# Optimization experiments

Hardware: AMD Instinct MI355X
Metric: run time of the kernel (lower is better)

The kernel has to match this reference:

```python
import jax, jax.numpy as jnp
import numpy as np

B, TM1, E, D = 512, 256, 256, 256  # batch, T-1, encoder_hidden, decoder_hidden


def setup_inputs() -> dict:
    key = jax.random.key(0)
    ks = jax.random.split(key, 10)
    s = 0.05
    return {
        "input_encoded": jax.random.normal(ks[0], (B, TM1, E), dtype=jnp.float32),
        "y_history": jax.random.normal(ks[1], (B, TM1, 1), dtype=jnp.float32),
        # attn_layer: Linear(2D+E -> E), Tanh, Linear(E -> 1)
        "attn_w1": jax.random.normal(ks[2], (E, 2 * D + E), dtype=jnp.float32) * s,
        "attn_b1": jnp.zeros((E,), jnp.float32),
        "attn_w2": jax.random.normal(ks[3], (1, E), dtype=jnp.float32) * s,
        "attn_b2": jnp.zeros((1,), jnp.float32),
        # LSTM cell: input_size=1, hidden=D
        "W_ih": jax.random.normal(ks[4], (4 * D, 1), dtype=jnp.float32) * s,
        "W_hh": jax.random.normal(ks[5], (4 * D, D), dtype=jnp.float32) * s,
        "b_ih": jnp.zeros((4 * D,), jnp.float32),
        "b_hh": jnp.zeros((4 * D,), jnp.float32),
        # fc: Linear(E+1 -> 1), weight init normal_()
        "fc_w": jax.random.normal(ks[6], (1, E + 1), dtype=jnp.float32),
        "fc_b": jnp.zeros((1,), jnp.float32),
        # fc_final: Linear(D+E -> 2) (probabilistic)
        "fcf_w": jax.random.normal(ks[7], (2, D + E), dtype=jnp.float32) * s,
        "fcf_b": jnp.zeros((2,), jnp.float32),
    }


def _forward(input_encoded, y_history, attn_w1, attn_b1, attn_w2, attn_b2,
             W_ih, W_hh, b_ih, b_hh, fc_w, fc_b, fcf_w, fcf_b):
    # Split attn first linear into [hidden|cell] part and encoder part.
    w1_hc = attn_w1[:, : 2 * D]   # (E, 2D)
    w1_enc = attn_w1[:, 2 * D:]   # (E, E)
    # Encoder projection is invariant across timesteps: compute once. (B,TM1,E)
    enc_proj = jnp.einsum("bte,fe->btf", input_encoded, w1_enc) + attn_b1

    def step(carry, y_t):
        h, c, _ = carry  # h,c: (B,D); y_t: (B,1)
        hc = jnp.concatenate([h, c], axis=1)                     # (B, 2D)
        pre = jnp.tanh(enc_proj + (hc @ w1_hc.T)[:, None, :])    # (B, TM1, E)
        scores = jnp.einsum("bte,oe->bto", pre, attn_w2)[..., 0] + attn_b2[0]  # (B, TM1)
        alpha = jax.nn.softmax(scores, axis=1)
        context = jnp.einsum("bt,bte->be", alpha, input_encoded)  # (B, E)
        y_tilde = jnp.concatenate([context, y_t], axis=1) @ fc_w.T + fc_b  # (B,1)
        # LSTM cell (torch gate order: i, f, g, o)
        gates = y_tilde @ W_ih.T + b_ih + h @ W_hh.T + b_hh  # (B, 4D)
        i, f, g, o = jnp.split(gates, 4, axis=1)
        i = jax.nn.sigmoid(i); f = jax.nn.sigmoid(f)
        g = jnp.tanh(g); o = jax.nn.sigmoid(o)
        c_new = f * c + i * g
        h_new = o * jnp.tanh(c_new)
        return (h_new, c_new, context), None

    h0 = jnp.zeros((input_encoded.shape[0], D), input_encoded.dtype)
    c0 = jnp.zeros_like(h0)
    ctx0 = jnp.zeros((input_encoded.shape[0], E), input_encoded.dtype)
    ys = jnp.transpose(y_history, (1, 0, 2))  # (TM1, B, 1)
    (h, c, context), _ = jax.lax.scan(step, (h0, c0, ctx0), ys)
    return jnp.concatenate([h, context], axis=1) @ fcf_w.T + fcf_b  # (B, 2)


def reference(input_encoded, y_history, attn_w1, attn_b1, attn_w2, attn_b2,
              W_ih, W_hh, b_ih, b_hh, fc_w, fc_b, fcf_w, fcf_b):
    return _forward(input_encoded, y_history, attn_w1, attn_b1, attn_w2, attn_b2,
                    W_ih, W_hh, b_ih, b_hh, fc_w, fc_b, fcf_w, fcf_b)
```

## Files before the change

### kernel.cpp

```cpp
#include <hip/hip_runtime.h>
#include <cstdint>
#include <cstddef>


typedef _Float16 half8 __attribute__((ext_vector_type(8)));
typedef _Float16 half4v __attribute__((ext_vector_type(4)));
typedef _Float16 half2v __attribute__((ext_vector_type(2)));

__device__ __forceinline__ float rcpf_(float x) { return __builtin_amdgcn_rcpf(x); }
__device__ __forceinline__ float sigmoidf_(float x) { return rcpf_(1.f + __expf(-x)); }
__device__ __forceinline__ float tanhf_(float x) { return 1.f - 2.f * rcpf_(1.f + __expf(2.f * x)); }

#if defined(__has_builtin)
#if __has_builtin(__builtin_amdgcn_fdot2)
#define HAS_FDOT2 1
#endif
#endif
#ifndef HAS_FDOT2
#define HAS_FDOT2 0
#endif

__device__ __forceinline__ float fdot2_(half2v a, half2v b, float c) {
#if HAS_FDOT2
  return __builtin_amdgcn_fdot2(a, b, c, false);
#else
  return fmaf((float)a[0], (float)b[0], fmaf((float)a[1], (float)b[1], c));
#endif
}

__device__ __forceinline__ float dot8_(half8 w, half8 h, float acc) {
  acc = fdot2_(__builtin_shufflevector(w, w, 0, 1), __builtin_shufflevector(h, h, 0, 1), acc);
  acc = fdot2_(__builtin_shufflevector(w, w, 2, 3), __builtin_shufflevector(h, h, 2, 3), acc);
  acc = fdot2_(__builtin_shufflevector(w, w, 4, 5), __builtin_shufflevector(h, h, 4, 5), acc);
  acc = fdot2_(__builtin_shufflevector(w, w, 6, 7), __builtin_shufflevector(h, h, 6, 7), acc);
  return acc;
}


__global__ void k_prep_wT(const float* __restrict__ w1, float* __restrict__ wT) {
  int id = blockIdx.x * 256 + threadIdx.x;
  int e = id >> 8, f = id & 255;
  wT[id] = w1[f * 768 + 512 + e];
}

__global__ void k_prep_xh(const float* __restrict__ x, _Float16* __restrict__ xh) {
  int id = blockIdx.x * 256 + threadIdx.x;
  float4 v = reinterpret_cast<const float4*>(x)[id];
  half4v h;
  h[0] = (_Float16)v.x; h[1] = (_Float16)v.y; h[2] = (_Float16)v.z; h[3] = (_Float16)v.w;
  reinterpret_cast<half4v*>(xh)[id] = h;
}

__global__ void k_prep_w1hcQ(const float* __restrict__ w1, _Float16* __restrict__ o) {
  int id = blockIdx.x * 256 + threadIdx.x;
  int m = id & 7, lane = (id >> 3) & 511, c = id >> 12;
  int e = lane >> 1, kh = lane & 1;
  o[id] = (_Float16)w1[e * 768 + kh * 256 + c * 8 + m];
}

__global__ void k_prep_whhG(const float* __restrict__ whh, _Float16* __restrict__ o) {
  int id = blockIdx.x * 256 + threadIdx.x;
  int m = id & 7, j = (id >> 3) & 1023, c = id >> 13;
  o[id] = (_Float16)whh[j * 256 + c * 8 + m];
}

__global__ __launch_bounds__(256) void k_xf(const float* __restrict__ x,
                                            const float* __restrict__ fcw,
                                            float* __restrict__ xf) {
  __shared__ float xl[16][256];
  __shared__ float fw[256];
  __shared__ float part[16][17];
  const int tid = threadIdx.x;
  const int m0 = blockIdx.x * 16;
  fw[tid] = fcw[tid];
#pragma unroll
  for (int r = 0; r < 16; ++r) xl[r][tid] = x[(size_t)(m0 + r) * 256 + tid];
  __syncthreads();
  int r = tid >> 4, p = tid & 15;
  float s = 0.f;
#pragma unroll
  for (int u = 0; u < 16; ++u) s = fmaf(xl[r][p * 16 + u], fw[p * 16 + u], s);
  part[r][p] = s;
  __syncthreads();
  if (tid < 16) {
    float t = 0.f;
#pragma unroll
    for (int p2 = 0; p2 < 16; ++p2) t += part[tid][p2];
    xf[m0 + tid] = t;
  }
}

__global__ __launch_bounds__(256) void k_encp(const float* __restrict__ x,
                                              const float* __restrict__ wT,
                                              const float* __restrict__ b1,
                                              _Float16* __restrict__ Ph2) {
  __shared__ __align__(16) float xl[16][256];
  const int tid = threadIdx.x;
  const int m0 = blockIdx.x * 16;
#pragma unroll
  for (int r = 0; r < 16; ++r) xl[r][tid] = x[(size_t)(m0 + r) * 256 + tid];
  __syncthreads();
  float acc[16];
#pragma unroll
  for (int r = 0; r < 16; ++r) acc[r] = 0.f;
  for (int e = 0; e < 256; e += 4) {
    float w0 = wT[(e + 0) * 256 + tid];
    float w1_ = wT[(e + 1) * 256 + tid];
    float w2_ = wT[(e + 2) * 256 + tid];
    float w3_ = wT[(e + 3) * 256 + tid];
#pragma unroll
    for (int r = 0; r < 16; ++r) {
      float4 xv = *reinterpret_cast<const float4*>(&xl[r][e]);
      acc[r] = fmaf(xv.x, w0, acc[r]);
      acc[r] = fmaf(xv.y, w1_, acc[r]);
      acc[r] = fmaf(xv.z, w2_, acc[r]);
      acc[r] = fmaf(xv.w, w3_, acc[r]);
    }
  }
  float bb = b1[tid];
  const int e = tid;
#pragma unroll
  for (int r = 0; r < 16; ++r) {
    int m = m0 + r, b = m >> 8, t = m & 255;
    float p = __expf(2.f * (acc[r] + bb));
    Ph2[((size_t)(b * 32 + (e >> 3)) * 256 + t) * 8 + (e & 7)] = (_Float16)p;
  }
}

#define SC1(pv, c) { \
  float4 qa = q4[2*(c)], wa = w4[2*(c)]; \
  sacc0 = fmaf(wa.x, rcpf_(fmaf((float)pv[0], qa.x, 1.f)), sacc0); \
  sacc1 = fmaf(wa.y, rcpf_(fmaf((float)pv[1], qa.y, 1.f)), sacc1); \
  sacc0 = fmaf(wa.z, rcpf_(fmaf((float)pv[2], qa.z, 1.f)), sacc0); \
  sacc1 = fmaf(wa.w, rcpf_(fmaf((float)pv[3], qa.w, 1.f)), sacc1); \
  float4 qb = q4[2*(c)+1], wb = w4[2*(c)+1]; \
  sacc0 = fmaf(wb.x, rcpf_(fmaf((float)pv[4], qb.x, 1.f)), sacc0); \
  sacc1 = fmaf(wb.y, rcpf_(fmaf((float)pv[5], qb.y, 1.f)), sacc1); \
  sacc0 = fmaf(wb.z, rcpf_(fmaf((float)pv[6], qb.z, 1.f)), sacc0); \
  sacc1 = fmaf(wb.w, rcpf_(fmaf((float)pv[7], qb.w, 1.f)), sacc1); }

__global__ __launch_bounds__(1024, 4) void k_scan(
    const _Float16* __restrict__ Ph2, const _Float16* __restrict__ xh,
    const _Float16* __restrict__ w1hcQ, const _Float16* __restrict__ whhG,
    const float* __restrict__ xf, const float* __restrict__ y_hist,
    const float* __restrict__ w2g, const float* __restrict__ Wih,
    const float* __restrict__ bih, const float* __restrict__ bhh,
    const float* __restrict__ fcw, const float* __restrict__ fcb,
    const float* __restrict__ fcfw, const float* __restrict__ fcfb,
    float* __restrict__ out) {
  __shared__ __align__(16) float hc[2][512];
  __shared__ __align__(16) _Float16 hcH[2][512];
  __shared__ __align__(16) float Qs[2][256];
  __shared__ __align__(16) float spart[2][2][256];
  __shared__ __align__(16) float ealpha[2][256];
  __shared__ __align__(16) float gfull[2][1024];
  __shared__ __align__(16) _Float16 PhL[2][14][256][8];
  __shared__ __align__(16) float w2l[256];
  __shared__ __align__(16) float Wihl[1024];
  __shared__ __align__(16) float bl[1024];
  __shared__ __align__(16) float xfL[2][256];
  __shared__ __align__(16) float yhL[2][256];
  __shared__ float redA[8], redB[8];

  const int tid = threadIdx.x;
  const int b0 = blockIdx.x * 2;
  const int lo = tid & 255;
  const int wv = tid >> 6, lane = tid & 63;

  ((float*)hc)[tid] = 0.f;
  ((_Float16*)hcH)[tid] = (_Float16)0.f;
  if (tid < 256) w2l[tid] = w2g[tid];
  Wihl[tid & 1023] = Wih[tid & 1023];
  bl[tid] = bih[tid] + bhh[tid];
  if (tid < 512) {
    int gi = tid >> 8, ti = tid & 255;
    xfL[gi][ti] = xf[(size_t)(b0 + gi) * 256 + ti];
    yhL[gi][ti] = y_hist[(size_t)(b0 + gi) * 256 + ti];
  }
  {
    half8* phl8 = reinterpret_cast<half8*>(&PhL[0][0][0][0]);
    const half8* ph8 = reinterpret_cast<const half8*>(Ph2);
#pragma unroll
    for (int u2 = 0; u2 < 7; ++u2) {
      int slot = u2 * 1024 + tid;
      int g = slot >= 3584;
      int rem = slot - g * 3584;
      int ci = rem >> 8;
      int t = rem & 255;
      int cc = (ci < 7) ? (2 * ci) : (16 + 2 * (ci - 7));
      phl8[slot] = ph8[((size_t)(b0 + g) * 32 + cc) * 256 + t];
    }
  }
  __syncthreads();
  float w2sum = 0.f;
  for (int e2 = 0; e2 < 256; ++e2) w2sum += w2l[e2];
  const float fcb0 = fcb[0];
  const float fcwy = fcw[256];

  const half8* wq2 = reinterpret_cast<const half8*>(w1hcQ) + tid;
  const int khq = tid & 1;
  const int ug = (tid - 512) & 511;
  const half8* wgJ = reinterpret_cast<const half8*>(whhG) + ug;
  const int gs = tid >> 9, eh = (tid >> 8) & 1;
  const half8* prow = reinterpret_cast<const half8*>(Ph2) +
                      ((size_t)((b0 + gs) * 32 + eh * 16)) * 256 + lo;
  const half8* phlR = reinterpret_cast<const half8*>(&PhL[0][0][0][0]) +
                      (gs * 14 + eh * 7) * 256 + lo;
  const int gp = (tid >> 8) & 1;

#pragma unroll 1
  for (int s = 0; s < 256; ++s) {
    if (tid < 512) {
      float a0 = 0.f, a1 = 0.f;
      const half8* hp0 = reinterpret_cast<const half8*>(&hcH[0][khq * 256]);
      const half8* hp1 = reinterpret_cast<const half8*>(&hcH[1][khq * 256]);
#pragma unroll 8
      for (int c = 0; c < 32; ++c) {
        half8 w = wq2[c * 512];
        a0 = dot8_(w, hp0[c], a0);
        a1 = dot8_(w, hp1[c], a1);
      }
      a0 += __shfl_xor(a0, 1);
      a1 += __shfl_xor(a1, 1);
      if (khq == 0) {
        int e = tid >> 1;
        Qs[0][e] = __expf(2.f * a0);
        Qs[1][e] = __expf(2.f * a1);
      }
    } else {
      float ac00 = 0.f, ac01 = 0.f, ac10 = 0.f, ac11 = 0.f;
      const half8* hg0 = reinterpret_cast<const half8*>(&hcH[0][0]);
      const half8* hg1 = reinterpret_cast<const half8*>(&hcH[1][0]);
#pragma unroll 4
      for (int c = 0; c < 32; ++c) {
        half8 h0 = hg0[c];
        half8 h1 = hg1[c];
        half8 w0 = wgJ[c * 1024];
        half8 w1v = wgJ[c * 1024 + 512];
        ac00 = dot8_(w0, h0, ac00);  ac01 = dot8_(w0, h1, ac01);
        ac10 = dot8_(w1v, h0, ac10); ac11 = dot8_(w1v, h1, ac11);
      }
      gfull[0][ug] = ac00;
      gfull[1][ug] = ac01;
      gfull[0][ug + 512] = ac10;
      gfull[1][ug + 512] = ac11;
    }
    __syncthreads();

    float sacc0 = 0.f, sacc1 = 0.f;
    {
      const float4* q4 = reinterpret_cast<const float4*>(&Qs[gs][eh * 128]);
      const float4* w4 = reinterpret_cast<const float4*>(&w2l[eh * 128]);
      half8 s1 = prow[1 * 256];
      half8 s3 = prow[3 * 256];
      half8 s5 = prow[5 * 256];
      half8 s7 = prow[7 * 256];
      half8 s9 = prow[9 * 256];
      half8 s11 = prow[11 * 256];
      half8 s13 = prow[13 * 256];
      half8 s14 = prow[14 * 256];
      half8 s15 = prow[15 * 256];
      { half8 l0 = phlR[0 * 256];  SC1(l0, 0) }
      { half8 l2 = phlR[1 * 256];  SC1(l2, 2) }
      { half8 l4 = phlR[2 * 256];  SC1(l4, 4) }
      { half8 l6 = phlR[3 * 256];  SC1(l6, 6) }
      { half8 l8 = phlR[4 * 256];  SC1(l8, 8) }
      { half8 la = phlR[5 * 256];  SC1(la, 10) }
      { half8 lc = phlR[6 * 256];  SC1(lc, 12) }
      SC1(s1, 1)  SC1(s3, 3)  SC1(s5, 5)  SC1(s7, 7)  SC1(s9, 9)
      SC1(s11, 11) SC1(s13, 13) SC1(s14, 14) SC1(s15, 15)
    }
    spart[eh][gs][lo] = sacc0 + sacc1;
    __syncthreads();

    if (tid < 512) {
      float sc = w2sum - 2.f * (spart[0][gp][lo] + spart[1][gp][lo]);
      float ea = __expf(sc);
      ealpha[gp][lo] = ea;
      float ef = ea * xfL[gp][lo];
      float es = ea;
#pragma unroll
      for (int off = 32; off > 0; off >>= 1) {
        es += __shfl_xor(es, off);
        ef += __shfl_xor(ef, off);
      }
      if (lane == 0) { redA[wv] = es; redB[wv] = ef; }
    }
    __syncthreads();

    if (tid < 512) {
      float es = (gp == 0) ? (redA[0] + redA[1] + redA[2] + redA[3])
                           : (redA[4] + redA[5] + redA[6] + redA[7]);
      float ef = (gp == 0) ? (redB[0] + redB[1] + redB[2] + redB[3])
                           : (redB[4] + redB[5] + redB[6] + redB[7]);
      float yt = ef * rcpf_(es) + fmaf(yhL[gp][s], fcwy, fcb0);
      float gi = fmaf(yt, Wihl[lo], bl[lo]) + gfull[gp][lo];
      float gf = fmaf(yt, Wihl[256 + lo], bl[256 + lo]) + gfull[gp][256 + lo];
      float gc = fmaf(yt, Wihl[512 + lo], bl[512 + lo]) + gfull[gp][512 + lo];
      float go = fmaf(yt, Wihl[768 + lo], bl[768 + lo]) + gfull[gp][768 + lo];
      float iv = sigmoidf_(gi), fv = sigmoidf_(gf), gv = tanhf_(gc), ov = sigmoidf_(go);
      float cold = hc[gp][256 + lo];
      float cn = fmaf(fv, cold, iv * gv);
      float hn = ov * tanhf_(cn);
      hc[gp][lo] = hn;
      hc[gp][256 + lo] = cn;
      hcH[gp][lo] = (_Float16)hn;
      hcH[gp][256 + lo] = (_Float16)cn;
    }
    __syncthreads();
  }

  const float rsA = rcpf_(redA[0] + redA[1] + redA[2] + redA[3]);
  const float rsB = rcpf_(redA[4] + redA[5] + redA[6] + redA[7]);

  float* cpartF = reinterpret_cast<float*>(&PhL[0][0][0][0]);
  {
    const int gc = tid >> 9, t16 = (tid >> 5) & 15, l5 = tid & 31;
    const half8* xrow = reinterpret_cast<const half8*>(xh) +
                        ((size_t)(b0 + gc) * 256 + t16 * 16) * 32 + l5;
    float acx[8];
#pragma unroll
    for (int m = 0; m < 8; ++m) acx[m] = 0.f;
#pragma unroll 4
    for (int it = 0; it < 16; ++it) {
      float al = ealpha[gc][t16 * 16 + it];
      half8 xv = xrow[it * 32];
#pragma unroll
      for (int m = 0; m < 8; ++m) acx[m] = fmaf(al, (float)xv[m], acx[m]);
    }
    float* dst = &cpartF[((gc * 16 + t16) * 256) + l5 * 8];
    *reinterpret_cast<float4*>(dst) = *reinterpret_cast<float4*>(&acx[0]);
    *reinterpret_cast<float4*>(dst + 4) = *reinterpret_cast<float4*>(&acx[4]);
  }
  __syncthreads();

  if (tid < 512) {
    float cv = 0.f;
#pragma unroll
    for (int u = 0; u < 16; ++u) cv += cpartF[((gp * 16 + u) * 256) + lo];
    cv *= (gp == 0) ? rsA : rsB;
    float hval = hc[gp][lo];
    float p0 = hval * fcfw[lo] + cv * fcfw[256 + lo];
    float p1 = hval * fcfw[512 + lo] + cv * fcfw[768 + lo];
#pragma unroll
    for (int off = 32; off > 0; off >>= 1) {
      p0 += __shfl_xor(p0, off);
      p1 += __shfl_xor(p1, off);
    }
    if (lane == 0) { redA[wv] = p0; redB[wv] = p1; }
  }
  __syncthreads();
  if (tid < 4) {
    int g2 = tid >> 1, o = tid & 1;
    const float* r = (o == 0) ? redA : redB;
    float v = fcfb[o] + r[g2 * 4 + 0] + r[g2 * 4 + 1] + r[g2 * 4 + 2] + r[g2 * 4 + 3];
    out[(b0 + g2) * 2 + o] = v;
  }
}

extern "C" void kernel_launch(void* const* d_in, const int* in_sizes, int n_in,
                              void* d_out, int out_size, void* d_ws, size_t ws_size,
                              hipStream_t stream) {
  (void)in_sizes; (void)n_in; (void)out_size; (void)ws_size;
  const float* x    = (const float*)d_in[0];
  const float* yh   = (const float*)d_in[1];
  const float* w1   = (const float*)d_in[2];
  const float* b1   = (const float*)d_in[3];
  const float* w2   = (const float*)d_in[4];
  const float* Wih  = (const float*)d_in[6];
  const float* Whh  = (const float*)d_in[7];
  const float* bih  = (const float*)d_in[8];
  const float* bhh  = (const float*)d_in[9];
  const float* fcw  = (const float*)d_in[10];
  const float* fcb  = (const float*)d_in[11];
  const float* fcfw = (const float*)d_in[12];
  const float* fcfb = (const float*)d_in[13];
  float* out = (float*)d_out;

  char* ws = (char*)d_ws;
  _Float16* Ph2   = (_Float16*)(ws);
  _Float16* xh    = (_Float16*)(ws + (size_t)67108864);
  float*    wT    = (float*)   (ws + (size_t)134217728);
  _Float16* w1hcQ = (_Float16*)(ws + (size_t)134479872);
  _Float16* whhG  = (_Float16*)(ws + (size_t)134742016);
  float*    xf    = (float*)   (ws + (size_t)135266304);

  k_prep_wT   <<<256,   256, 0, stream>>>(w1, wT);
  k_prep_xh   <<<32768, 256, 0, stream>>>(x, xh);
  k_prep_w1hcQ<<<512,   256, 0, stream>>>(w1, w1hcQ);
  k_prep_whhG <<<1024,  256, 0, stream>>>(Whh, whhG);
  k_xf        <<<8192,  256, 0, stream>>>(x, fcw, xf);
  k_encp      <<<8192,  256, 0, stream>>>(x, wT, b1, Ph2);
  k_scan      <<<256,  1024, 0, stream>>>(Ph2, xh, w1hcQ, whhG, xf, yh, w2, Wih,
                                          bih, bhh, fcw, fcb, fcfw, fcfb, out);
}
```

Measured before the change: 3.722 ms.

## Overlap attention scores with split W_hh gate matvec across thread halves

The W_hh gate matvec is split into two halves. The second half now runs on the upper 512 threads at the same time as the attention-score pass, which is done entirely by the lower 512 threads over all 256 encoder features. This removes the spart partial-score buffer and one block barrier per timestep. The LDS copy of the projected encoder is widened to hold all even chunks, and the c half of hcH is padded to reduce bank conflicts. In exchange, each score thread does twice as much rcp-heavy work and issues more global loads, which lengthens the score critical path and pushes LDS use close to the limit.

```diff
diff --git a/kernel.cpp b/kernel.cpp
--- a/kernel.cpp
+++ b/kernel.cpp
@@ -149,12 +149,11 @@
     const float* __restrict__ fcfw, const float* __restrict__ fcfb,
     float* __restrict__ out) {
   __shared__ __align__(16) float hc[2][512];
-  __shared__ __align__(16) _Float16 hcH[2][512];
+  __shared__ __align__(16) _Float16 hcH[2][520];
   __shared__ __align__(16) float Qs[2][256];
-  __shared__ __align__(16) float spart[2][2][256];
   __shared__ __align__(16) float ealpha[2][256];
   __shared__ __align__(16) float gfull[2][1024];
-  __shared__ __align__(16) _Float16 PhL[2][14][256][8];
+  __shared__ __align__(16) _Float16 PhL[2][16][256][8];
   __shared__ __align__(16) float w2l[256];
   __shared__ __align__(16) float Wihl[1024];
   __shared__ __align__(16) float bl[1024];
@@ -168,7 +167,10 @@
   const int wv = tid >> 6, lane = tid & 63;
 
   ((float*)hc)[tid] = 0.f;
-  ((_Float16*)hcH)[tid] = (_Float16)0.f;
+  if (tid < 520) {
+    hcH[0][tid] = (_Float16)0.f;
+    hcH[1][tid] = (_Float16)0.f;
+  }
   if (tid < 256) w2l[tid] = w2g[tid];
   Wihl[tid & 1023] = Wih[tid & 1023];
   bl[tid] = bih[tid] + bhh[tid];
@@ -181,13 +183,13 @@
     half8* phl8 = reinterpret_cast<half8*>(&PhL[0][0][0][0]);
     const half8* ph8 = reinterpret_cast<const half8*>(Ph2);
 #pragma unroll
-    for (int u2 = 0; u2 < 7; ++u2) {
+    for (int u2 = 0; u2 < 8; ++u2) {
       int slot = u2 * 1024 + tid;
-      int g = slot >= 3584;
-      int rem = slot - g * 3584;
+      int g = slot >= 4096;
+      int rem = slot - g * 4096;
       int ci = rem >> 8;
       int t = rem & 255;
-      int cc = (ci < 7) ? (2 * ci) : (16 + 2 * (ci - 7));
+      int cc = 2 * ci;
       phl8[slot] = ph8[((size_t)(b0 + g) * 32 + cc) * 256 + t];
     }
   }
@@ -201,19 +203,19 @@
   const int khq = tid & 1;
   const int ug = (tid - 512) & 511;
   const half8* wgJ = reinterpret_cast<const half8*>(whhG) + ug;
-  const int gs = tid >> 9, eh = (tid >> 8) & 1;
+  const int gs = (tid >> 8) & 1;
   const half8* prow = reinterpret_cast<const half8*>(Ph2) +
-                      ((size_t)((b0 + gs) * 32 + eh * 16)) * 256 + lo;
+                      ((size_t)((b0 + gs) * 32)) * 256 + lo;
   const half8* phlR = reinterpret_cast<const half8*>(&PhL[0][0][0][0]) +
-                      (gs * 14 + eh * 7) * 256 + lo;
+                      (gs * 16) * 256 + lo;
   const int gp = (tid >> 8) & 1;
 
 #pragma unroll 1
   for (int s = 0; s < 256; ++s) {
     if (tid < 512) {
       float a0 = 0.f, a1 = 0.f;
-      const half8* hp0 = reinterpret_cast<const half8*>(&hcH[0][khq * 256]);
-      const half8* hp1 = reinterpret_cast<const half8*>(&hcH[1][khq * 256]);
+      const half8* hp0 = reinterpret_cast<const half8*>(&hcH[0][khq * 264]);
+      const half8* hp1 = reinterpret_cast<const half8*>(&hcH[1][khq * 264]);
 #pragma unroll 8
       for (int c = 0; c < 32; ++c) {
         half8 w = wq2[c * 512];
@@ -232,7 +234,7 @@
       const half8* hg0 = reinterpret_cast<const half8*>(&hcH[0][0]);
       const half8* hg1 = reinterpret_cast<const half8*>(&hcH[1][0]);
 #pragma unroll 4
-      for (int c = 0; c < 32; ++c) {
+      for (int c = 0; c < 16; ++c) {
         half8 h0 = hg0[c];
         half8 h1 = hg1[c];
         half8 w0 = wgJ[c * 1024];
@@ -247,37 +249,44 @@
     }
     __syncthreads();
 
-    float sacc0 = 0.f, sacc1 = 0.f;
-    {
-      const float4* q4 = reinterpret_cast<const float4*>(&Qs[gs][eh * 128]);
-      const float4* w4 = reinterpret_cast<const float4*>(&w2l[eh * 128]);
-      half8 s1 = prow[1 * 256];
-      half8 s3 = prow[3 * 256];
-      half8 s5 = prow[5 * 256];
-      half8 s7 = prow[7 * 256];
-      half8 s9 = prow[9 * 256];
-      half8 s11 = prow[11 * 256];
-      half8 s13 = prow[13 * 256];
-      half8 s14 = prow[14 * 256];
-      half8 s15 = prow[15 * 256];
-      { half8 l0 = phlR[0 * 256];  SC1(l0, 0) }
-      { half8 l2 = phlR[1 * 256];  SC1(l2, 2) }
-      { half8 l4 = phlR[2 * 256];  SC1(l4, 4) }
-      { half8 l6 = phlR[3 * 256];  SC1(l6, 6) }
-      { half8 l8 = phlR[4 * 256];  SC1(l8, 8) }
-      { half8 la = phlR[5 * 256];  SC1(la, 10) }
-      { half8 lc = phlR[6 * 256];  SC1(lc, 12) }
-      SC1(s1, 1)  SC1(s3, 3)  SC1(s5, 5)  SC1(s7, 7)  SC1(s9, 9)
-      SC1(s11, 11) SC1(s13, 13) SC1(s14, 14) SC1(s15, 15)
-    }
-    spart[eh][gs][lo] = sacc0 + sacc1;
-    __syncthreads();
-
     if (tid < 512) {
-      float sc = w2sum - 2.f * (spart[0][gp][lo] + spart[1][gp][lo]);
+      float sacc0 = 0.f, sacc1 = 0.f;
+      {
+        const float4* q4 = reinterpret_cast<const float4*>(&Qs[gs][0]);
+        const float4* w4 = reinterpret_cast<const float4*>(&w2l[0]);
+        half8 p1_ = prow[1 * 256];   half8 p3_ = prow[3 * 256];
+        half8 p5_ = prow[5 * 256];   half8 p7_ = prow[7 * 256];
+        half8 p9_ = prow[9 * 256];   half8 p11_ = prow[11 * 256];
+        half8 p13_ = prow[13 * 256]; half8 p15_ = prow[15 * 256];
+        half8 p17_ = prow[17 * 256]; half8 p19_ = prow[19 * 256];
+        half8 p21_ = prow[21 * 256]; half8 p23_ = prow[23 * 256];
+        half8 p25_ = prow[25 * 256]; half8 p27_ = prow[27 * 256];
+        half8 p29_ = prow[29 * 256]; half8 p31_ = prow[31 * 256];
+        { half8 l = phlR[0 * 256];   SC1(l, 0) }
+        { half8 l = phlR[1 * 256];   SC1(l, 2) }
+        { half8 l = phlR[2 * 256];   SC1(l, 4) }
+        { half8 l = phlR[3 * 256];   SC1(l, 6) }
+        { half8 l = phlR[4 * 256];   SC1(l, 8) }
+        { half8 l = phlR[5 * 256];   SC1(l, 10) }
+        { half8 l = phlR[6 * 256];   SC1(l, 12) }
+        { half8 l = phlR[7 * 256];   SC1(l, 14) }
+        { half8 l = phlR[8 * 256];   SC1(l, 16) }
+        { half8 l = phlR[9 * 256];   SC1(l, 18) }
+        { half8 l = phlR[10 * 256];  SC1(l, 20) }
+        { half8 l = phlR[11 * 256];  SC1(l, 22) }
+        { half8 l = phlR[12 * 256];  SC1(l, 24) }
+        { half8 l = phlR[13 * 256];  SC1(l, 26) }
+        { half8 l = phlR[14 * 256];  SC1(l, 28) }
+        { half8 l = phlR[15 * 256];  SC1(l, 30) }
+        SC1(p1_, 1)   SC1(p3_, 3)   SC1(p5_, 5)   SC1(p7_, 7)
+        SC1(p9_, 9)   SC1(p11_, 11) SC1(p13_, 13) SC1(p15_, 15)
+        SC1(p17_, 17) SC1(p19_, 19) SC1(p21_, 21) SC1(p23_, 23)
+        SC1(p25_, 25) SC1(p27_, 27) SC1(p29_, 29) SC1(p31_, 31)
+      }
+      float sc = w2sum - 2.f * (sacc0 + sacc1);
       float ea = __expf(sc);
-      ealpha[gp][lo] = ea;
-      float ef = ea * xfL[gp][lo];
+      ealpha[gs][lo] = ea;
+      float ef = ea * xfL[gs][lo];
       float es = ea;
 #pragma unroll
       for (int off = 32; off > 0; off >>= 1) {
@@ -285,6 +294,23 @@
         ef += __shfl_xor(ef, off);
       }
       if (lane == 0) { redA[wv] = es; redB[wv] = ef; }
+    } else {
+      float ac00 = 0.f, ac01 = 0.f, ac10 = 0.f, ac11 = 0.f;
+      const half8* hg0 = reinterpret_cast<const half8*>(&hcH[0][0]);
+      const half8* hg1 = reinterpret_cast<const half8*>(&hcH[1][0]);
+#pragma unroll 4
+      for (int c = 16; c < 32; ++c) {
+        half8 h0 = hg0[c];
+        half8 h1 = hg1[c];
+        half8 w0 = wgJ[c * 1024];
+        half8 w1v = wgJ[c * 1024 + 512];
+        ac00 = dot8_(w0, h0, ac00);  ac01 = dot8_(w0, h1, ac01);
+        ac10 = dot8_(w1v, h0, ac10); ac11 = dot8_(w1v, h1, ac11);
+      }
+      gfull[0][ug] += ac00;
+      gfull[1][ug] += ac01;
+      gfull[0][ug + 512] += ac10;
+      gfull[1][ug + 512] += ac11;
     }
     __syncthreads();
 
@@ -305,7 +331,7 @@
       hc[gp][lo] = hn;
       hc[gp][256 + lo] = cn;
       hcH[gp][lo] = (_Float16)hn;
-      hcH[gp][256 + lo] = (_Float16)cn;
+      hcH[gp][264 + lo] = (_Float16)cn;
     }
     __syncthreads();
   }
```

Measured after the change: 5.858 ms. +57.4%, slower.
